# Kernel tuning notes

Hardware: AMD Instinct MI355X
Metric: run time of the kernel (lower is better)

## Reference

```python
import jax, jax.numpy as jnp
import numpy as np

# Dims derived from the module: len(vocab)=V, E=V-4, bidirectional 2-layer LSTM.
V, E, H, L = 1028, 1024, 1024, 2
B, T = 16, 512
BOS, PAD = 1, 0  # vocab.bos_idx, vocab.pad_idx


def setup_inputs() -> dict:
    key = jax.random.key(0)
    ks = jax.random.split(key, 10)
    sc = 1.0 / np.sqrt(H)  # PyTorch LSTM init scale
    inputs = jax.random.randint(ks[0], (B, T), 0, V, dtype=jnp.int32)
    emb = (jax.random.normal(ks[1], (V, E), jnp.float32) * 0.02).at[PAD].set(0.0)
    # [dir, 4H, in_dim] weights; layer 0 consumes E, layer 1 consumes 2H (bidir concat).
    w_ih_l0 = jax.random.uniform(ks[2], (2, 4 * H, E), jnp.float32, -sc, sc)
    w_hh_l0 = jax.random.uniform(ks[3], (2, 4 * H, H), jnp.float32, -sc, sc)
    b_ih_l0 = jax.random.uniform(ks[4], (2, 4 * H), jnp.float32, -sc, sc)
    b_hh_l0 = jax.random.uniform(ks[5], (2, 4 * H), jnp.float32, -sc, sc)
    w_ih_l1 = jax.random.uniform(ks[6], (2, 4 * H, 2 * H), jnp.float32, -sc, sc)
    w_hh_l1 = jax.random.uniform(ks[7], (2, 4 * H, H), jnp.float32, -sc, sc)
    b_ih_l1 = jax.random.uniform(ks[8], (2, 4 * H), jnp.float32, -sc, sc)
    b_hh_l1 = jax.random.uniform(ks[9], (2, 4 * H), jnp.float32, -sc, sc)
    return {"inputs": inputs, "emb": emb,
            "w_ih_l0": w_ih_l0, "w_hh_l0": w_hh_l0, "b_ih_l0": b_ih_l0, "b_hh_l0": b_hh_l0,
            "w_ih_l1": w_ih_l1, "w_hh_l1": w_hh_l1, "b_ih_l1": b_ih_l1, "b_hh_l1": b_hh_l1}


def lstm_cell(x, h, c, wih, whh, b):
    # PyTorch gate order: i, f, g, o
    g = x @ wih.T + h @ whh.T + b
    i, f, gg, o = jnp.split(g, 4, axis=-1)
    c2 = jax.nn.sigmoid(f) * c + jax.nn.sigmoid(i) * jnp.tanh(gg)
    h2 = jax.nn.sigmoid(o) * jnp.tanh(c2)
    return h2, c2


def reference(inputs, emb, w_ih_l0, w_hh_l0, b_ih_l0, b_hh_l0,
              w_ih_l1, w_hh_l1, b_ih_l1, b_hh_l1):
    Bb, Tt = inputs.shape
    # step 0 consumes BOS; steps i>=1 consume inputs[:, i] (inputs[:,0] is never used)
    toks = jnp.concatenate([jnp.full((Bb, 1), BOS, inputs.dtype), inputs[:, 1:]], axis=1)
    xs = emb[toks].transpose(1, 0, 2)  # [T, B, E]; dropout is eval-mode identity
    b0 = b_ih_l0 + b_hh_l0
    b1 = b_ih_l1 + b_hh_l1
    h0 = jnp.zeros((4, Bb, H), xs.dtype)  # [l0f, l0b, l1f, l1b]
    c0 = jnp.zeros((4, Bb, H), xs.dtype)

    def step(carry, x):
        h, c = carry
        # length-1 sequence: forward and backward directions see the same token
        h0f, c0f = lstm_cell(x, h[0], c[0], w_ih_l0[0], w_hh_l0[0], b0[0])
        h0b, c0b = lstm_cell(x, h[1], c[1], w_ih_l0[1], w_hh_l0[1], b0[1])
        x1 = jnp.concatenate([h0f, h0b], axis=-1)  # [B, 2H]
        h1f, c1f = lstm_cell(x1, h[2], c[2], w_ih_l1[0], w_hh_l1[0], b1[0])
        h1b, c1b = lstm_cell(x1, h[3], c[3], w_ih_l1[1], w_hh_l1[1], b1[1])
        out = jnp.concatenate([h1f, h1b], axis=-1)  # [B, 2H]
        return (jnp.stack([h0f, h0b, h1f, h1b]), jnp.stack([c0f, c0b, c1f, c1b])), out

    _, outs = jax.lax.scan(step, (h0, c0), xs)
    return outs.transpose(1, 0, 2)  # [B, T, 2H]
```

## Files before the change

### kernel.cpp

```cpp
#include <hip/hip_runtime.h>
#include <hip/hip_bf16.h>
#include <stdint.h>


#define TT 512
#define HH 1024

typedef __bf16 bf16x8 __attribute__((ext_vector_type(8)));
typedef float f32x4 __attribute__((ext_vector_type(4)));
typedef unsigned int u32;
typedef unsigned short u16;

#define MFMA __builtin_amdgcn_mfma_f32_16x16x32_bf16

#define OFS_B0    4096ul
#define OFS_B1    36864ul
#define OFS_X     69632ul
#define OFS_WIH0  16846848ul
#define OFS_WHH0  33624064ul
#define OFS_W1    50401280ul
#define OFS_H0    100732928ul
#define OFS_H1    134287360ul

__device__ inline u16 f2b(float f){
  union { float f; u32 u; } x{f};
  return (u16)((x.u + 0x7FFFu + ((x.u >> 16) & 1u)) >> 16);
}
__device__ inline float sigm(float x){ return 1.f/(1.f + __expf(-x)); }
__device__ inline float tanh_(float x){ return 2.f*sigm(2.f*x) - 1.f; }

__device__ inline void g_store32(u32* p, u32 v){
  asm volatile("global_store_dword %0, %1, off sc0 sc1" :: "v"(p), "v"(v) : "memory");
}

#define G_LOAD8(A, P) asm volatile( \
  "global_load_dwordx4 %0, %8, off sc0 sc1\n\t" \
  "global_load_dwordx4 %1, %8, off offset:64 sc0 sc1\n\t" \
  "global_load_dwordx4 %2, %8, off offset:128 sc0 sc1\n\t" \
  "global_load_dwordx4 %3, %8, off offset:192 sc0 sc1\n\t" \
  "global_load_dwordx4 %4, %8, off offset:256 sc0 sc1\n\t" \
  "global_load_dwordx4 %5, %8, off offset:320 sc0 sc1\n\t" \
  "global_load_dwordx4 %6, %8, off offset:384 sc0 sc1\n\t" \
  "global_load_dwordx4 %7, %8, off offset:448 sc0 sc1\n\t" \
  "s_waitcnt vmcnt(0)" \
  : "=&v"(A[0]), "=&v"(A[1]), "=&v"(A[2]), "=&v"(A[3]), \
    "=&v"(A[4]), "=&v"(A[5]), "=&v"(A[6]), "=&v"(A[7]) \
  : "v"(P) : "memory")

#define G_LOAD4_ISSUE(A, P) asm volatile( \
  "global_load_dwordx4 %0, %4, off sc0 sc1\n\t" \
  "global_load_dwordx4 %1, %4, off offset:64 sc0 sc1\n\t" \
  "global_load_dwordx4 %2, %4, off offset:128 sc0 sc1\n\t" \
  "global_load_dwordx4 %3, %4, off offset:192 sc0 sc1" \
  : "=&v"(A[0]), "=&v"(A[1]), "=&v"(A[2]), "=&v"(A[3]) \
  : "v"(P) : "memory")
#define G_WAIT4(A) asm volatile("s_waitcnt vmcnt(0)" \
  : "+v"(A[0]), "+v"(A[1]), "+v"(A[2]), "+v"(A[3]) :: "memory")
#define G_LOAD4W(A, P) asm volatile( \
  "global_load_dwordx4 %0, %4, off sc0 sc1\n\t" \
  "global_load_dwordx4 %1, %4, off offset:64 sc0 sc1\n\t" \
  "global_load_dwordx4 %2, %4, off offset:128 sc0 sc1\n\t" \
  "global_load_dwordx4 %3, %4, off offset:192 sc0 sc1\n\t" \
  "s_waitcnt vmcnt(0)" \
  : "=&v"(A[0]), "=&v"(A[1]), "=&v"(A[2]), "=&v"(A[3]) \
  : "v"(P) : "memory")

__device__ inline int frag_ok(const f32x4 v){
  uint4 u = __builtin_bit_cast(uint4, v);
  return (u.x != 0xFFFFFFFFu) & (u.y != 0xFFFFFFFFu) &
         (u.z != 0xFFFFFFFFu) & (u.w != 0xFFFFFFFFu);
}

__global__ void k_bias(const float* __restrict__ a0, const float* __restrict__ a1,
                       const float* __restrict__ a2, const float* __restrict__ a3,
                       float* __restrict__ b0, float* __restrict__ b1,
                       unsigned long long* __restrict__ h1z){
  int i = blockIdx.x*256 + threadIdx.x;
  if (i < 8192){ b0[i] = a0[i] + a1[i]; b1[i] = a2[i] + a3[i]; h1z[i] = 0ull; }
}

__global__ void k_embed(const int* __restrict__ inputs, const float* __restrict__ emb,
                        u16* __restrict__ X){
  int row = blockIdx.x;
  int t = row >> 4, b = row & 15;
  int tok = (t == 0) ? 1 : inputs[b*TT + t];
  const float4* src = (const float4*)(emb + (size_t)tok*HH);
  float4 v = src[threadIdx.x];
  ushort4 o = make_ushort4(f2b(v.x), f2b(v.y), f2b(v.z), f2b(v.w));
  ((ushort4*)X)[(size_t)row*256 + threadIdx.x] = o;
}

__global__ void k_pack(const float* __restrict__ sA, const float* __restrict__ sB,
                       int KA, int KB, u16* __restrict__ dst){
  int K = KA + KB, KS = K >> 5;
  long idx = (long)blockIdx.x*256 + threadIdx.x;
  long total = 2L*64*4*KS*64;
  if (idx >= total) return;
  int l = (int)(idx & 63);
  long r = idx >> 6;
  int ks = (int)(r % KS); r /= KS;
  int g  = (int)(r & 3);  r >>= 2;
  int jb = (int)(r & 63); r >>= 6;
  int cell = (int)r;
  int n  = g*1024 + jb*16 + (l & 15);
  int k0 = ks*32 + ((l >> 4) << 3);
  const float* s; int kl;
  if (k0 < KA){ s = sA + (long)(cell*4096 + n)*KA; kl = k0; }
  else        { s = sB + (long)(cell*4096 + n)*KB; kl = k0 - KA; }
  float4 f0 = *(const float4*)(s + kl);
  float4 f1 = *(const float4*)(s + kl + 4);
  union { u16 v[8]; int4 q; } o;
  o.v[0]=f2b(f0.x); o.v[1]=f2b(f0.y); o.v[2]=f2b(f0.z); o.v[3]=f2b(f0.w);
  o.v[4]=f2b(f1.x); o.v[5]=f2b(f1.y); o.v[6]=f2b(f1.z); o.v[7]=f2b(f1.w);
  long d = ((((long)cell*64 + jb)*4 + g)*KS + ks)*64 + l;
  ((int4*)dst)[d] = o.q;
}

__global__ __launch_bounds__(512, 2)
void k_fused(const u16* __restrict__ Wih0p, const u16* __restrict__ Whh0p,
             const u16* __restrict__ W1p, const float* __restrict__ b0,
             const float* __restrict__ b1, const u16* __restrict__ Xb,
             u16* h0_all, u16* h1r, float* __restrict__ out)
{
  extern __shared__ char smem[];
  float*  gl   = (float*)smem;
  f32x4*  wlds = (f32x4*)(smem + 32768);

  const int tid  = threadIdx.x;
  const int wv   = tid >> 6, l = tid & 63;
  const int rowA = l & 15;
  const int kq8  = (l >> 4) * 8;
  const int layer = blockIdx.x >> 7;
  const int bid   = blockIdx.x & 127;
  const int cell  = bid >> 6, jb = bid & 63;
  const int b_ = tid >> 4, j = tid & 15;

  float bias[4];
  {
    const float* bb = (layer == 0 ? b0 : b1) + cell*4096 + jb*16 + rowA;
    #pragma unroll
    for (int g = 0; g < 4; g++) bias[g] = (wv == 0) ? bb[g*1024] : 0.f;
  }
  float creg = 0.f;

  if (layer == 0){
    f32x4 w[4][8];
    {
      const f32x4* src = (const f32x4*)(wv < 4 ? Wih0p : Whh0p)
                       + ((long)(cell*64 + jb)*4)*32*64 + l;
      #pragma unroll
      for (int g = 0; g < 4; g++)
        #pragma unroll
        for (int i = 0; i < 8; i++)
          w[g][i] = src[((long)g*32 + (wv & 3)*8 + i)*64];
    }
    #pragma unroll
    for (int g = 0; g < 4; g++)
      #pragma unroll
      for (int i = 0; i < 8; i++) asm volatile("" : "+v"(w[g][i]));
    __syncthreads();

    u32* hdst = (u32*)h0_all;
    const int ko = (wv & 3)*256;

    for (int t = 0; t < TT; t++){
      f32x4 acc[4];
      #pragma unroll
      for (int g = 0; g < 4; g++) acc[g] = (f32x4){bias[g],bias[g],bias[g],bias[g]};
      if (wv < 4){
        const u16* A = Xb + ((long)t*16 + rowA)*1024 + ko + kq8;
        f32x4 Af[8];
        #pragma unroll
        for (int i = 0; i < 8; i++) Af[i] = *(const f32x4*)(A + i*32);
        #pragma unroll
        for (int i = 0; i < 8; i++)
          #pragma unroll
          for (int g = 0; g < 4; g++)
            acc[g] = MFMA(__builtin_bit_cast(bf16x8, Af[i]),
                          __builtin_bit_cast(bf16x8, w[g][i]), acc[g], 0, 0, 0);
      } else if (t > 0){
        const u16* A = h0_all + (((long)(t-1)*2 + cell)*16 + rowA)*1024 + ko + kq8;
        f32x4 Af[8];
        for (;;){
          G_LOAD8(Af, A);
          int ok = 1;
          #pragma unroll
          for (int i = 0; i < 8; i++) ok &= frag_ok(Af[i]);
          if (__all(ok)) break;
        }
        #pragma unroll
        for (int i = 0; i < 8; i++)
          #pragma unroll
          for (int g = 0; g < 4; g++)
            acc[g] = MFMA(__builtin_bit_cast(bf16x8, Af[i]),
                          __builtin_bit_cast(bf16x8, w[g][i]), acc[g], 0, 0, 0);
      }
      {
        int r0 = (l >> 4)*4, cj = l & 15;
        #pragma unroll
        for (int g = 0; g < 4; g++)
          #pragma unroll
          for (int i2 = 0; i2 < 4; i2++)
            gl[wv*1024 + g*256 + (r0+i2)*16 + cj] = acc[g][i2];
      }
      __syncthreads();
      if (tid < 256){
        float s0=0.f, s1=0.f, s2=0.f, s3=0.f;
        #pragma unroll
        for (int wq = 0; wq < 8; wq++){
          s0 += gl[wq*1024 + tid];
          s1 += gl[wq*1024 + 256 + tid];
          s2 += gl[wq*1024 + 512 + tid];
          s3 += gl[wq*1024 + 768 + tid];
        }
        float c2 = sigm(s1)*creg + sigm(s0)*tanh_(s2);
        float h2 = sigm(s3)*tanh_(c2);
        creg = c2;
        u32 lo = f2b(h2), hi = __shfl_down(lo, 1);
        if (!(tid & 1)){
          long idx = ((((long)t*2 + cell)*16 + b_)*1024 + jb*16 + j) >> 1;
          g_store32(hdst + idx, lo | (hi << 16));
        }
      }
      __syncthreads();
    }
  } else {
    f32x4 wh0[4][8];
    f32x4 wh1[4];
    {
      const f32x4* src = (const f32x4*)W1p + ((long)(cell*64 + jb)*4)*96*64 + l;
      #pragma unroll
      for (int g = 0; g < 4; g++){
        #pragma unroll
        for (int i = 0; i < 8; i++)
          wh0[g][i] = src[((long)g*96 + wv*8 + i)*64];
        wh1[g] = src[((long)g*96 + 64 + wv*4)*64];
      }
      const f32x4* wb = (const f32x4*)W1p + ((long)(cell*64 + jb)*4)*96*64;
      for (int i = tid; i < 6144; i += 512){
        int g = i / 1536, r = (i % 1536) >> 6, ll = i & 63;
        int ksl = 64 + (r/3)*4 + (r%3) + 1;
        wlds[i] = wb[((long)g*96 + ksl)*64 + ll];
      }
    }
    #pragma unroll
    for (int g = 0; g < 4; g++){
      #pragma unroll
      for (int i = 0; i < 8; i++) asm volatile("" : "+v"(wh0[g][i]));
      asm volatile("" : "+v"(wh1[g]));
    }
    __syncthreads();

    u32* h1d = (u32*)h1r;

    for (int t = 0; t < TT; t++){
      if (tid < 256 && !(tid & 1)){
        long idx = ((((long)((t+1)&3)*2 + cell)*16 + b_)*1024 + jb*16 + j) >> 1;
        g_store32(h1d + idx, 0xFFFFFFFFu);
      }
      f32x4 Bf[4];
      const u16* Ah = h1r + (((long)((t+3)&3)*2 + cell)*16 + rowA)*1024
                    + wv*128 + kq8;
      G_LOAD4_ISSUE(Bf, Ah);
      f32x4 acc[4];
      #pragma unroll
      for (int g = 0; g < 4; g++) acc[g] = (f32x4){bias[g],bias[g],bias[g],bias[g]};
      {
        const u16* A = h0_all + ((long)t*32 + (wv>>2)*16 + rowA)*1024
                     + (wv & 3)*256 + kq8;
        f32x4 Af[8];
        for (;;){
          G_LOAD8(Af, A);
          int ok = 1;
          #pragma unroll
          for (int i = 0; i < 8; i++) ok &= frag_ok(Af[i]);
          if (__all(ok)) break;
        }
        #pragma unroll
        for (int i = 0; i < 8; i++)
          #pragma unroll
          for (int g = 0; g < 4; g++)
            acc[g] = MFMA(__builtin_bit_cast(bf16x8, Af[i]),
                          __builtin_bit_cast(bf16x8, wh0[g][i]), acc[g], 0, 0, 0);
      }
      G_WAIT4(Bf);
      for (;;){
        int ok = 1;
        #pragma unroll
        for (int i = 0; i < 4; i++) ok &= frag_ok(Bf[i]);
        if (__all(ok)) break;
        G_LOAD4W(Bf, Ah);
      }
      #pragma unroll
      for (int i = 0; i < 4; i++)
        #pragma unroll
        for (int g = 0; g < 4; g++){
          f32x4 bw = (i == 0) ? wh1[g] : wlds[(g*24 + wv*3 + (i-1))*64 + l];
          acc[g] = MFMA(__builtin_bit_cast(bf16x8, Bf[i]),
                        __builtin_bit_cast(bf16x8, bw), acc[g], 0, 0, 0);
        }
      {
        int r0 = (l >> 4)*4, cj = l & 15;
        #pragma unroll
        for (int g = 0; g < 4; g++)
          #pragma unroll
          for (int i2 = 0; i2 < 4; i2++)
            gl[wv*1024 + g*256 + (r0+i2)*16 + cj] = acc[g][i2];
      }
      __syncthreads();
      if (tid < 256){
        float s0=0.f, s1=0.f, s2=0.f, s3=0.f;
        #pragma unroll
        for (int wq = 0; wq < 8; wq++){
          s0 += gl[wq*1024 + tid];
          s1 += gl[wq*1024 + 256 + tid];
          s2 += gl[wq*1024 + 512 + tid];
          s3 += gl[wq*1024 + 768 + tid];
        }
        float c2 = sigm(s1)*creg + sigm(s0)*tanh_(s2);
        float h2 = sigm(s3)*tanh_(c2);
        creg = c2;
        out[((long)b_*TT + t)*2048 + cell*1024 + jb*16 + j] = h2;
        u32 lo = f2b(h2), hi = __shfl_down(lo, 1);
        if (!(tid & 1)){
          long idx = ((((long)(t & 3)*2 + cell)*16 + b_)*1024 + jb*16 + j) >> 1;
          g_store32(h1d + idx, lo | (hi << 16));
        }
      }
      __syncthreads();
    }
  }
}

extern "C" void kernel_launch(void* const* d_in, const int* in_sizes, int n_in,
                              void* d_out, int out_size, void* d_ws, size_t ws_size,
                              hipStream_t stream){
  const int*   inputs = (const int*)d_in[0];
  const float* emb    = (const float*)d_in[1];
  const float* wih0   = (const float*)d_in[2];
  const float* whh0   = (const float*)d_in[3];
  const float* bih0   = (const float*)d_in[4];
  const float* bhh0   = (const float*)d_in[5];
  const float* wih1   = (const float*)d_in[6];
  const float* whh1   = (const float*)d_in[7];
  const float* bih1   = (const float*)d_in[8];
  const float* bhh1   = (const float*)d_in[9];
  float* out = (float*)d_out;
  char* ws = (char*)d_ws;

  float* b0    = (float*)(ws + OFS_B0);
  float* b1    = (float*)(ws + OFS_B1);
  u16*   Xb    = (u16*)(ws + OFS_X);
  u16*   Wih0p = (u16*)(ws + OFS_WIH0);
  u16*   Whh0p = (u16*)(ws + OFS_WHH0);
  u16*   W1p   = (u16*)(ws + OFS_W1);
  u16*   h0a   = (u16*)(ws + OFS_H0);
  u16*   h1r   = (u16*)(ws + OFS_H1);
  unsigned long long* h1z = (unsigned long long*)(ws + OFS_H1 + 196608ul);

  hipMemsetAsync(ws + OFS_H0, 0xFF, 33554432ul, stream);
  hipMemsetAsync(ws + OFS_H1, 0xFF, 196608ul, stream);
  k_bias <<<32,   256, 0, stream>>>(bih0, bhh0, bih1, bhh1, b0, b1, h1z);
  k_embed<<<8192, 256, 0, stream>>>(inputs, emb, Xb);
  k_pack <<<4096, 256, 0, stream>>>(wih0, (const float*)0, 1024, 0, Wih0p);
  k_pack <<<4096, 256, 0, stream>>>(whh0, (const float*)0, 1024, 0, Whh0p);
  k_pack <<<12288,256, 0, stream>>>(wih1, whh1, 2048, 1024, W1p);

  const int smem_bytes = 32768 + 98304;
  hipFuncSetAttribute(reinterpret_cast<const void*>(&k_fused),
                      hipFuncAttributeMaxDynamicSharedMemorySize, smem_bytes);
  k_fused<<<256, 512, smem_bytes, stream>>>(Wih0p, Whh0p, W1p, b0, b1, Xb,
                                            h0a, h1r, out);
}
```

Before: 3.043 ms.

## Prefetch layer-0 recurrent h into LDS asynchronously while gate waves compute

```diff
diff --git a/kernel.cpp b/kernel.cpp
--- a/kernel.cpp
+++ b/kernel.cpp
@@ -12,6 +12,7 @@
 typedef unsigned short u16;
 
 #define MFMA __builtin_amdgcn_mfma_f32_16x16x32_bf16
+#define RAW_BAR() asm volatile("s_waitcnt lgkmcnt(0)\n\ts_barrier" ::: "memory")
 
 #define OFS_B0    4096ul
 #define OFS_B1    36864ul
@@ -31,6 +32,12 @@
 
 __device__ inline void g_store32(u32* p, u32 v){
   asm volatile("global_store_dword %0, %1, off sc0 sc1" :: "v"(p), "v"(v) : "memory");
+}
+
+__device__ inline void async_ld16(const u16* g, char* l){
+  __builtin_amdgcn_global_load_lds(
+      (const __attribute__((address_space(1))) void*)g,
+      (__attribute__((address_space(3))) void*)l, 16, 0, 0x11);
 }
 
 #define G_LOAD8(A, P) asm volatile( \
@@ -69,6 +76,16 @@
   uint4 u = __builtin_bit_cast(uint4, v);
   return (u.x != 0xFFFFFFFFu) & (u.y != 0xFFFFFFFFu) &
          (u.z != 0xFFFFFFFFu) & (u.w != 0xFFFFFFFFu);
+}
+
+__device__ inline void poll8(f32x4* Af, const u16* A){
+  for (;;){
+    G_LOAD8(Af, A);
+    int ok = 1;
+    #pragma unroll
+    for (int i = 0; i < 8; i++) ok &= frag_ok(Af[i]);
+    if (__all(ok)) return;
+  }
 }
 
 __global__ void k_bias(const float* __restrict__ a0, const float* __restrict__ a1,
@@ -162,6 +179,8 @@
 
     u32* hdst = (u32*)h0_all;
     const int ko = (wv & 3)*256;
+    const f32x4* sv = (const f32x4*)(smem + 32768 + (wv & 3)*8192);
+    char* sb = smem + 32768 + (wv & 3)*8192;
 
     for (int t = 0; t < TT; t++){
       f32x4 acc[4];
@@ -181,13 +200,13 @@
       } else if (t > 0){
         const u16* A = h0_all + (((long)(t-1)*2 + cell)*16 + rowA)*1024 + ko + kq8;
         f32x4 Af[8];
-        for (;;){
-          G_LOAD8(Af, A);
-          int ok = 1;
-          #pragma unroll
-          for (int i = 0; i < 8; i++) ok &= frag_ok(Af[i]);
-          if (__all(ok)) break;
-        }
+        asm volatile("s_waitcnt vmcnt(0)" ::: "memory");
+        #pragma unroll
+        for (int i = 0; i < 8; i++) Af[i] = sv[i*64 + l];
+        int ok = 1;
+        #pragma unroll
+        for (int i = 0; i < 8; i++) ok &= frag_ok(Af[i]);
+        if (!__all(ok)) poll8(Af, A);
         #pragma unroll
         for (int i = 0; i < 8; i++)
           #pragma unroll
@@ -203,7 +222,7 @@
           for (int i2 = 0; i2 < 4; i2++)
             gl[wv*1024 + g*256 + (r0+i2)*16 + cj] = acc[g][i2];
       }
-      __syncthreads();
+      RAW_BAR();
       if (tid < 256){
         float s0=0.f, s1=0.f, s2=0.f, s3=0.f;
         #pragma unroll
@@ -221,8 +240,13 @@
           long idx = ((((long)t*2 + cell)*16 + b_)*1024 + jb*16 + j) >> 1;
           g_store32(hdst + idx, lo | (hi << 16));
         }
-      }
-      __syncthreads();
+      } else if (t < TT-1){
+        __builtin_amdgcn_s_sleep(12);
+        const u16* An = h0_all + (((long)t*2 + cell)*16 + rowA)*1024 + ko + kq8;
+        #pragma unroll
+        for (int i = 0; i < 8; i++) async_ld16(An + i*32, sb + i*1024);
+      }
+      RAW_BAR();
     }
   } else {
     f32x4 wh0[4][8];
@@ -254,14 +278,14 @@
     u32* h1d = (u32*)h1r;
 
     for (int t = 0; t < TT; t++){
-      if (tid < 256 && !(tid & 1)){
-        long idx = ((((long)((t+1)&3)*2 + cell)*16 + b_)*1024 + jb*16 + j) >> 1;
-        g_store32(h1d + idx, 0xFFFFFFFFu);
-      }
       f32x4 Bf[4];
       const u16* Ah = h1r + (((long)((t+3)&3)*2 + cell)*16 + rowA)*1024
                     + wv*128 + kq8;
       G_LOAD4_ISSUE(Bf, Ah);
+      if (tid < 256 && !(tid & 1)){
+        long idx = ((((long)((t+1)&3)*2 + cell)*16 + b_)*1024 + jb*16 + j) >> 1;
+        g_store32(h1d + idx, 0xFFFFFFFFu);
+      }
       f32x4 acc[4];
       #pragma unroll
       for (int g = 0; g < 4; g++) acc[g] = (f32x4){bias[g],bias[g],bias[g],bias[g]};
@@ -269,13 +293,7 @@
         const u16* A = h0_all + ((long)t*32 + (wv>>2)*16 + rowA)*1024
                      + (wv & 3)*256 + kq8;
         f32x4 Af[8];
-        for (;;){
-          G_LOAD8(Af, A);
-          int ok = 1;
-          #pragma unroll
-          for (int i = 0; i < 8; i++) ok &= frag_ok(Af[i]);
-          if (__all(ok)) break;
-        }
+        poll8(Af, A);
         #pragma unroll
         for (int i = 0; i < 8; i++)
           #pragma unroll
@@ -284,12 +302,16 @@
                           __builtin_bit_cast(bf16x8, wh0[g][i]), acc[g], 0, 0, 0);
       }
       G_WAIT4(Bf);
-      for (;;){
+      {
         int ok = 1;
         #pragma unroll
         for (int i = 0; i < 4; i++) ok &= frag_ok(Bf[i]);
-        if (__all(ok)) break;
-        G_LOAD4W(Bf, Ah);
+        while (!__all(ok)){
+          G_LOAD4W(Bf, Ah);
+          ok = 1;
+          #pragma unroll
+          for (int i = 0; i < 4; i++) ok &= frag_ok(Bf[i]);
+        }
       }
       #pragma unroll
       for (int i = 0; i < 4; i++)
@@ -307,7 +329,7 @@
           for (int i2 = 0; i2 < 4; i2++)
             gl[wv*1024 + g*256 + (r0+i2)*16 + cj] = acc[g][i2];
       }
-      __syncthreads();
+      RAW_BAR();
       if (tid < 256){
         float s0=0.f, s1=0.f, s2=0.f, s3=0.f;
         #pragma unroll
@@ -327,7 +349,7 @@
           g_store32(h1d + idx, lo | (hi << 16));
         }
       }
-      __syncthreads();
+      RAW_BAR();
     }
   }
 }
```

Result: slower. 3.402 ms (+11.8%).

## Add per-block progress flags to replace heavy sentinel polling of hidden states

Applied to the files above, without the earlier changes.

```diff
diff --git a/kernel.cpp b/kernel.cpp
--- a/kernel.cpp
+++ b/kernel.cpp
@@ -13,6 +13,7 @@
 
 #define MFMA __builtin_amdgcn_mfma_f32_16x16x32_bf16
 
+#define OFS_FLAGS 0ul
 #define OFS_B0    4096ul
 #define OFS_B1    36864ul
 #define OFS_X     69632ul
@@ -31,6 +32,12 @@
 
 __device__ inline void g_store32(u32* p, u32 v){
   asm volatile("global_store_dword %0, %1, off sc0 sc1" :: "v"(p), "v"(v) : "memory");
+}
+__device__ inline u32 g_ld32(const u32* p){
+  u32 v;
+  asm volatile("global_load_dword %0, %1, off sc0 sc1\n\t"
+               "s_waitcnt vmcnt(0)" : "=&v"(v) : "v"(p) : "memory");
+  return v;
 }
 
 #define G_LOAD8(A, P) asm volatile( \
@@ -69,6 +76,23 @@
   uint4 u = __builtin_bit_cast(uint4, v);
   return (u.x != 0xFFFFFFFFu) & (u.y != 0xFFFFFFFFu) &
          (u.z != 0xFFFFFFFFu) & (u.w != 0xFFFFFFFFu);
+}
+
+__device__ inline void flag_wait(const u32* f, int li, u32 tgt){
+  for (;;){
+    u32 c = g_ld32(f + li);
+    if (__all((int)(c >= tgt))) return;
+  }
+}
+
+__device__ inline void poll8(f32x4* Af, const u16* A){
+  for (;;){
+    G_LOAD8(Af, A);
+    int ok = 1;
+    #pragma unroll
+    for (int i = 0; i < 8; i++) ok &= frag_ok(Af[i]);
+    if (__all(ok)) return;
+  }
 }
 
 __global__ void k_bias(const float* __restrict__ a0, const float* __restrict__ a1,
@@ -120,7 +144,7 @@
 void k_fused(const u16* __restrict__ Wih0p, const u16* __restrict__ Whh0p,
              const u16* __restrict__ W1p, const float* __restrict__ b0,
              const float* __restrict__ b1, const u16* __restrict__ Xb,
-             u16* h0_all, u16* h1r, float* __restrict__ out)
+             u16* h0_all, u16* h1r, float* __restrict__ out, u32* flags)
 {
   extern __shared__ char smem[];
   float*  gl   = (float*)smem;
@@ -161,6 +185,8 @@
     __syncthreads();
 
     u32* hdst = (u32*)h0_all;
+    u32* myf  = flags + cell*64 + jb;
+    const u32* flr = flags + cell*64 + (wv & 3)*16;
     const int ko = (wv & 3)*256;
 
     for (int t = 0; t < TT; t++){
@@ -181,12 +207,13 @@
       } else if (t > 0){
         const u16* A = h0_all + (((long)(t-1)*2 + cell)*16 + rowA)*1024 + ko + kq8;
         f32x4 Af[8];
-        for (;;){
-          G_LOAD8(Af, A);
-          int ok = 1;
-          #pragma unroll
-          for (int i = 0; i < 8; i++) ok &= frag_ok(Af[i]);
-          if (__all(ok)) break;
+        G_LOAD8(Af, A);
+        int ok = 1;
+        #pragma unroll
+        for (int i = 0; i < 8; i++) ok &= frag_ok(Af[i]);
+        if (!__all(ok)){
+          flag_wait(flr, l & 15, (u32)t);
+          poll8(Af, A);
         }
         #pragma unroll
         for (int i = 0; i < 8; i++)
@@ -223,6 +250,7 @@
         }
       }
       __syncthreads();
+      if (tid == 0) g_store32(myf, (u32)(t+1));
     }
   } else {
     f32x4 wh0[4][8];
@@ -252,16 +280,19 @@
     __syncthreads();
 
     u32* h1d = (u32*)h1r;
+    u32* myf = flags + (2 + cell)*64 + jb;
+    const u32* fl0 = flags + (wv >> 2)*64 + (wv & 3)*16;
+    const u32* flh = flags + (2 + cell)*64 + wv*8;
 
     for (int t = 0; t < TT; t++){
-      if (tid < 256 && !(tid & 1)){
-        long idx = ((((long)((t+1)&3)*2 + cell)*16 + b_)*1024 + jb*16 + j) >> 1;
-        g_store32(h1d + idx, 0xFFFFFFFFu);
-      }
       f32x4 Bf[4];
       const u16* Ah = h1r + (((long)((t+3)&3)*2 + cell)*16 + rowA)*1024
                     + wv*128 + kq8;
       G_LOAD4_ISSUE(Bf, Ah);
+      if (tid < 256 && !(tid & 1)){
+        long idx = ((((long)((t+1)&3)*2 + cell)*16 + b_)*1024 + jb*16 + j) >> 1;
+        g_store32(h1d + idx, 0xFFFFFFFFu);
+      }
       f32x4 acc[4];
       #pragma unroll
       for (int g = 0; g < 4; g++) acc[g] = (f32x4){bias[g],bias[g],bias[g],bias[g]};
@@ -269,12 +300,13 @@
         const u16* A = h0_all + ((long)t*32 + (wv>>2)*16 + rowA)*1024
                      + (wv & 3)*256 + kq8;
         f32x4 Af[8];
-        for (;;){
-          G_LOAD8(Af, A);
-          int ok = 1;
-          #pragma unroll
-          for (int i = 0; i < 8; i++) ok &= frag_ok(Af[i]);
-          if (__all(ok)) break;
+        G_LOAD8(Af, A);
+        int ok = 1;
+        #pragma unroll
+        for (int i = 0; i < 8; i++) ok &= frag_ok(Af[i]);
+        if (!__all(ok)){
+          flag_wait(fl0, l & 15, (u32)(t+1));
+          poll8(Af, A);
         }
         #pragma unroll
         for (int i = 0; i < 8; i++)
@@ -284,12 +316,20 @@
                           __builtin_bit_cast(bf16x8, wh0[g][i]), acc[g], 0, 0, 0);
       }
       G_WAIT4(Bf);
-      for (;;){
+      {
         int ok = 1;
         #pragma unroll
         for (int i = 0; i < 4; i++) ok &= frag_ok(Bf[i]);
-        if (__all(ok)) break;
-        G_LOAD4W(Bf, Ah);
+        if (!__all(ok)){
+          flag_wait(flh, l & 7, (u32)t);
+          for (;;){
+            G_LOAD4W(Bf, Ah);
+            ok = 1;
+            #pragma unroll
+            for (int i = 0; i < 4; i++) ok &= frag_ok(Bf[i]);
+            if (__all(ok)) break;
+          }
+        }
       }
       #pragma unroll
       for (int i = 0; i < 4; i++)
@@ -328,6 +368,7 @@
         }
       }
       __syncthreads();
+      if (tid == 0) g_store32(myf, (u32)(t+1));
     }
   }
 }
@@ -348,6 +389,7 @@
   float* out = (float*)d_out;
   char* ws = (char*)d_ws;
 
+  u32*   flags = (u32*)(ws + OFS_FLAGS);
   float* b0    = (float*)(ws + OFS_B0);
   float* b1    = (float*)(ws + OFS_B1);
   u16*   Xb    = (u16*)(ws + OFS_X);
@@ -358,6 +400,7 @@
   u16*   h1r   = (u16*)(ws + OFS_H1);
   unsigned long long* h1z = (unsigned long long*)(ws + OFS_H1 + 196608ul);
 
+  hipMemsetAsync(flags, 0, 4096, stream);
   hipMemsetAsync(ws + OFS_H0, 0xFF, 33554432ul, stream);
   hipMemsetAsync(ws + OFS_H1, 0xFF, 196608ul, stream);
   k_bias <<<32,   256, 0, stream>>>(bih0, bhh0, bih1, bhh1, b0, b1, h1z);
@@ -370,5 +413,5 @@
   hipFuncSetAttribute(reinterpret_cast<const void*>(&k_fused),
                       hipFuncAttributeMaxDynamicSharedMemorySize, smem_bytes);
   k_fused<<<256, 512, smem_bytes, stream>>>(Wih0p, Whh0p, W1p, b0, b1, Xb,
-                                            h0a, h1r, out);
-}
+                                            h0a, h1r, out, flags);
+}
```

Result: no change. 3.056 ms (+0.4%).
